# Kernel optimization log

Hardware: AMD Instinct MI355X
Metric: run time of the kernel (lower is better)

The kernel has to match this reference:

```python
import jax, jax.numpy as jnp
import numpy as np

B, L, DM = 4, 512, 512
NH, DK, DV = 8, 64, 64  # NOTE: module's view puts d_k as the 'heads' axis, n_head as feature axis
EPS = 1e-6


def setup_inputs() -> dict:
    key = jax.random.key(0)
    ks = jax.random.split(key, 12)
    xav = lambda k, shp: jax.random.uniform(k, shp, jnp.float32, -1.0, 1.0) * np.sqrt(6.0 / (shp[0] + shp[1]))
    return {
        "q": jax.random.normal(ks[0], (B, L, DM), jnp.float32),
        "k": jax.random.normal(ks[1], (B, L, DM), jnp.float32),
        "v": jax.random.normal(ks[2], (B, L, DM), jnp.float32),
        "similarity": jax.random.normal(ks[3], (B, DK, L, L), jnp.float32),
        "Wq": xav(ks[4], (NH * DK, DM)),
        "Wk": xav(ks[5], (NH * DK, DM)),
        "Wv": xav(ks[6], (NH * DV, DM)),
        "Wfc": xav(ks[7], (DM, NH * DV)),
        "bfc": jnp.zeros((DM,), jnp.float32),
        "ln_g": jnp.ones((DM,), jnp.float32),
        "ln_b": jnp.zeros((DM,), jnp.float32),
    }


def reference(q, k, v, similarity, Wq, Wk, Wv, Wfc, bfc, ln_g, ln_b):
    b, l, dm = q.shape
    residual = q
    # pre-LayerNorm applied to q only (normalize_before=True)
    mu = jnp.mean(q, axis=-1, keepdims=True)
    var = jnp.mean(jnp.square(q - mu), axis=-1, keepdims=True)
    qn = (q - mu) / jnp.sqrt(var + EPS) * ln_g + ln_b
    # projections, then view(b, l, d_k, n_head).transpose(1,2) -> [b, d_k, l, n_head]
    Q = (qn @ Wq.T).reshape(b, l, DK, NH).transpose(0, 2, 1, 3)
    K = (k @ Wk.T).reshape(b, l, DK, NH).transpose(0, 2, 1, 3)
    V = (v @ Wv.T).reshape(b, l, DK, NH).transpose(0, 2, 1, 3)
    temp = jnp.asarray(DK ** 0.5, q.dtype)
    # bias-augmented scaled dot-product attention: scores [b, d_k, l, l]
    scores = jnp.einsum('bhqe,bhke->bhqk', Q, K) / temp + similarity
    attn = jax.nn.softmax(scores, axis=-1)  # dropout omitted (eval mode)
    out = jnp.einsum('bhqk,bhke->bhqe', attn, V)  # [b, d_k, l, n_head]
    out = out.transpose(0, 2, 1, 3).reshape(b, l, DK * NH)
    out = out @ Wfc.T + bfc + residual
    return out, attn
```

## Files before the change

kernel.cpp:

```cpp
#include <hip/hip_runtime.h>

#define DMODEL 512
#define LSEQ   512
#define BATCH  4
#define NTOK   2048

typedef __attribute__((ext_vector_type(8))) short bf8;
typedef __attribute__((ext_vector_type(4))) float f4;
typedef __attribute__((ext_vector_type(4))) unsigned short us4;
typedef __attribute__((ext_vector_type(8))) unsigned short us8;

__device__ __forceinline__ unsigned short bf16_rne(float f) {
  unsigned int u = __float_as_uint(f);
  u += 0x7FFFu + ((u >> 16) & 1u);
  return (unsigned short)(u >> 16);
}
__device__ __forceinline__ void split2(float f, unsigned short& h, unsigned short& l) {
  unsigned short hh = bf16_rne(f);
  float fh = __uint_as_float(((unsigned int)hh) << 16);
  h = hh;
  l = bf16_rne(f - fh);
}

__global__ __launch_bounds__(256) void ln_kernel(const float* __restrict__ q,
    const float* __restrict__ gamma, const float* __restrict__ beta,
    unsigned short* __restrict__ qh, unsigned short* __restrict__ qlo) {
  int row = blockIdx.x;
  const float* x = q + (size_t)row * DMODEL;
  int t = threadIdx.x;
  float v0 = x[t];
  float v1 = x[t + 256];
  float s  = v0 + v1;
  float ss = v0 * v0 + v1 * v1;
  #pragma unroll
  for (int o = 32; o >= 1; o >>= 1) {
    s  += __shfl_down(s, o);
    ss += __shfl_down(ss, o);
  }
  __shared__ float ls[4], lss[4];
  __shared__ float smu, srstd;
  int wid = t >> 6, lane = t & 63;
  if (lane == 0) { ls[wid] = s; lss[wid] = ss; }
  __syncthreads();
  if (t == 0) {
    float S  = ls[0] + ls[1] + ls[2] + ls[3];
    float SS = lss[0] + lss[1] + lss[2] + lss[3];
    float mu  = S * (1.0f / DMODEL);
    float var = SS * (1.0f / DMODEL) - mu * mu;
    smu = mu;
    srstd = rsqrtf(var + 1e-6f);
  }
  __syncthreads();
  float mu = smu, rstd = srstd;
  float n0 = (v0 - mu) * rstd * gamma[t]       + beta[t];
  float n1 = (v1 - mu) * rstd * gamma[t + 256] + beta[t + 256];
  unsigned short h, l;
  size_t base = (size_t)row * DMODEL;
  split2(n0, h, l); qh[base + t] = h;       qlo[base + t] = l;
  split2(n1, h, l); qh[base + t + 256] = h; qlo[base + t + 256] = l;
}

__global__ __launch_bounds__(256) void conv_kernel(
    const float* __restrict__ k, const float* __restrict__ v,
    const float* __restrict__ Wq, const float* __restrict__ Wk,
    const float* __restrict__ Wv, const float* __restrict__ Wf,
    unsigned short* __restrict__ kh, unsigned short* __restrict__ kl,
    unsigned short* __restrict__ vh, unsigned short* __restrict__ vl,
    unsigned short* __restrict__ Wqh, unsigned short* __restrict__ Wql,
    unsigned short* __restrict__ Wkh, unsigned short* __restrict__ Wkl,
    unsigned short* __restrict__ Wvh, unsigned short* __restrict__ Wvl,
    unsigned short* __restrict__ Wfh, unsigned short* __restrict__ Wfl) {
  const float* src; unsigned short* dh; unsigned short* dl; int n;
  switch (blockIdx.y) {
    case 0:  src = k;  dh = kh;  dl = kl;  n = NTOK * DMODEL; break;
    case 1:  src = v;  dh = vh;  dl = vl;  n = NTOK * DMODEL; break;
    case 2:  src = Wq; dh = Wqh; dl = Wql; n = DMODEL * DMODEL; break;
    case 3:  src = Wk; dh = Wkh; dl = Wkl; n = DMODEL * DMODEL; break;
    case 4:  src = Wv; dh = Wvh; dl = Wvl; n = DMODEL * DMODEL; break;
    default: src = Wf; dh = Wfh; dl = Wfl; n = DMODEL * DMODEL; break;
  }
  int idx = blockIdx.x * 1024 + threadIdx.x * 4;
  if (idx >= n) return;
  float4 f = *(const float4*)(src + idx);
  us4 oh, ol;
  unsigned short h, l;
  split2(f.x, h, l); oh[0] = h; ol[0] = l;
  split2(f.y, h, l); oh[1] = h; ol[1] = l;
  split2(f.z, h, l); oh[2] = h; ol[2] = l;
  split2(f.w, h, l); oh[3] = h; ol[3] = l;
  *(us4*)(dh + idx) = oh;
  *(us4*)(dl + idx) = ol;
}

__device__ __forceinline__ void mfma_gemm_body(
    const unsigned short* __restrict__ Ah, const unsigned short* __restrict__ Al,
    const unsigned short* __restrict__ Wh, const unsigned short* __restrict__ Wl,
    float* __restrict__ C, const float* __restrict__ bias, const float* __restrict__ resid) {
  const int t = threadIdx.x;
  const int w = t >> 6, lane = t & 63;
  const int wm = w >> 1, wn = w & 1;
  const int r0 = blockIdx.y * 64 + wm * 32;
  const int c0 = blockIdx.x * 64 + wn * 32;
  const int lr = lane & 15, quad = lane >> 4;
  f4 acc[2][2] = {};
  for (int k0 = 0; k0 < DMODEL; k0 += 32) {
    const int ko = k0 + quad * 8;
    bf8 ah[2], al[2], bh[2], bl[2];
    #pragma unroll
    for (int mi = 0; mi < 2; mi++) {
      const size_t off = (size_t)(r0 + mi * 16 + lr) * DMODEL + ko;
      ah[mi] = *(const bf8*)(Ah + off);
      al[mi] = *(const bf8*)(Al + off);
    }
    #pragma unroll
    for (int ni = 0; ni < 2; ni++) {
      const size_t off = (size_t)(c0 + ni * 16 + lr) * DMODEL + ko;
      bh[ni] = *(const bf8*)(Wh + off);
      bl[ni] = *(const bf8*)(Wl + off);
    }
    #pragma unroll
    for (int mi = 0; mi < 2; mi++)
      #pragma unroll
      for (int ni = 0; ni < 2; ni++) {
        acc[mi][ni] = __builtin_amdgcn_mfma_f32_16x16x32_bf16(al[mi], bh[ni], acc[mi][ni], 0, 0, 0);
        acc[mi][ni] = __builtin_amdgcn_mfma_f32_16x16x32_bf16(ah[mi], bl[ni], acc[mi][ni], 0, 0, 0);
        acc[mi][ni] = __builtin_amdgcn_mfma_f32_16x16x32_bf16(ah[mi], bh[ni], acc[mi][ni], 0, 0, 0);
      }
  }
  #pragma unroll
  for (int mi = 0; mi < 2; mi++)
    #pragma unroll
    for (int ni = 0; ni < 2; ni++)
      #pragma unroll
      for (int r = 0; r < 4; r++) {
        int row = r0 + mi * 16 + quad * 4 + r;
        int col = c0 + ni * 16 + lr;
        float o = acc[mi][ni][r];
        if (bias)  o += bias[col];
        if (resid) o += resid[(size_t)row * DMODEL + col];
        C[(size_t)row * DMODEL + col] = o;
      }
}

__global__ __launch_bounds__(256) void proj_mfma(
    const unsigned short* __restrict__ qnh, const unsigned short* __restrict__ qnl,
    const unsigned short* __restrict__ kh, const unsigned short* __restrict__ kl,
    const unsigned short* __restrict__ vh, const unsigned short* __restrict__ vl,
    const unsigned short* __restrict__ Wqh, const unsigned short* __restrict__ Wql,
    const unsigned short* __restrict__ Wkh, const unsigned short* __restrict__ Wkl,
    const unsigned short* __restrict__ Wvh, const unsigned short* __restrict__ Wvl,
    float* __restrict__ Qp, float* __restrict__ Kp, float* __restrict__ Vp) {
  const unsigned short *Ah, *Al, *Wh, *Wl; float* C;
  if (blockIdx.z == 0)      { Ah = qnh; Al = qnl; Wh = Wqh; Wl = Wql; C = Qp; }
  else if (blockIdx.z == 1) { Ah = kh;  Al = kl;  Wh = Wkh; Wl = Wkl; C = Kp; }
  else                      { Ah = vh;  Al = vl;  Wh = Wvh; Wl = Wvl; C = Vp; }
  mfma_gemm_body(Ah, Al, Wh, Wl, C, nullptr, nullptr);
}

__global__ __launch_bounds__(256) void fc_mfma(
    const unsigned short* __restrict__ AOh, const unsigned short* __restrict__ AOl,
    const unsigned short* __restrict__ Wfh, const unsigned short* __restrict__ Wfl,
    const float* __restrict__ bfc, const float* __restrict__ resid,
    float* __restrict__ out) {
  mfma_gemm_body(AOh, AOl, Wfh, Wfl, out, bfc, resid);
}

__global__ __launch_bounds__(256, 3) void attn2_kernel(
    const float* __restrict__ Qp, const float* __restrict__ Kp, const float* __restrict__ Vp,
    const float* __restrict__ sim, float* __restrict__ attn_out,
    unsigned short* __restrict__ AOh, unsigned short* __restrict__ AOl) {
  __shared__ float Vt[8][516];
  __shared__ float Qs[64][8];
  const int qt = blockIdx.x, dk = blockIdx.y, b = blockIdx.z;
  const int t = threadIdx.x;
  const float* Vbase = Vp + (size_t)b * LSEQ * DMODEL + dk * 8;
  #pragma unroll
  for (int it = 0; it < 16; it++) {
    int idx = it * 256 + t;
    int l = idx >> 3, j = idx & 7;
    Vt[j][l] = Vbase[(size_t)l * DMODEL + j];
  }
  const float* Qbase = Qp + ((size_t)b * LSEQ + qt * 64) * DMODEL + dk * 8;
  #pragma unroll
  for (int it = 0; it < 2; it++) {
    int idx = it * 256 + t;
    int l = idx >> 3, j = idx & 7;
    Qs[l][j] = Qbase[(size_t)l * DMODEL + j];
  }
  const int lane = t & 63, w = t >> 6;
  const float* Kbase = Kp + (size_t)b * LSEQ * DMODEL + dk * 8;
  float Kr[2][8][4];
  #pragma unroll
  for (int c = 0; c < 2; c++)
    #pragma unroll
    for (int s = 0; s < 4; s++) {
      const float* kr = Kbase + (size_t)(c * 256 + lane * 4 + s) * DMODEL;
      float4 a  = *(const float4*)kr;
      float4 bb = *(const float4*)(kr + 4);
      Kr[c][0][s] = a.x;  Kr[c][1][s] = a.y;  Kr[c][2][s] = a.z;  Kr[c][3][s] = a.w;
      Kr[c][4][s] = bb.x; Kr[c][5][s] = bb.y; Kr[c][6][s] = bb.z; Kr[c][7][s] = bb.w;
    }
  __syncthreads();

  for (int qi = 0; qi < 16; qi++) {
    const int ql = w * 16 + qi;
    const int q  = qt * 64 + ql;
    const size_t rowoff = (((size_t)(b * 64 + dk) * LSEQ) + q) * LSEQ;
    float4 sv0 = *(const float4*)(sim + rowoff + lane * 4);
    float4 sv1 = *(const float4*)(sim + rowoff + 256 + lane * 4);
    float svf[2][4] = {{sv0.x, sv0.y, sv0.z, sv0.w}, {sv1.x, sv1.y, sv1.z, sv1.w}};
    float qreg[8];
    #pragma unroll
    for (int j = 0; j < 8; j++) qreg[j] = Qs[ql][j];
    float sc[2][4];
    #pragma unroll
    for (int c = 0; c < 2; c++)
      #pragma unroll
      for (int s = 0; s < 4; s++) {
        float d = 0.0f;
        #pragma unroll
        for (int j = 0; j < 8; j++) d = fmaf(qreg[j], Kr[c][j][s], d);
        sc[c][s] = fmaf(d, 0.125f, svf[c][s]);
      }
    float m = sc[0][0];
    #pragma unroll
    for (int c = 0; c < 2; c++)
      #pragma unroll
      for (int s = 0; s < 4; s++) m = fmaxf(m, sc[c][s]);
    #pragma unroll
    for (int o = 1; o < 64; o <<= 1) m = fmaxf(m, __shfl_xor(m, o));
    float p[2][4]; float sum = 0.0f;
    #pragma unroll
    for (int c = 0; c < 2; c++)
      #pragma unroll
      for (int s = 0; s < 4; s++) { p[c][s] = __expf(sc[c][s] - m); sum += p[c][s]; }
    #pragma unroll
    for (int o = 1; o < 64; o <<= 1) sum += __shfl_xor(sum, o);
    const float r = 1.0f / sum;
    #pragma unroll
    for (int c = 0; c < 2; c++)
      #pragma unroll
      for (int s = 0; s < 4; s++) p[c][s] *= r;
    float4 st0 = {p[0][0], p[0][1], p[0][2], p[0][3]};
    float4 st1 = {p[1][0], p[1][1], p[1][2], p[1][3]};
    *(float4*)(attn_out + rowoff + lane * 4) = st0;
    *(float4*)(attn_out + rowoff + 256 + lane * 4) = st1;
    float pv[8];
    #pragma unroll
    for (int j = 0; j < 8; j++) {
      float acc = 0.0f;
      #pragma unroll
      for (int c = 0; c < 2; c++) {
        float4 vv = *(const float4*)&Vt[j][c * 256 + lane * 4];
        acc = fmaf(p[c][0], vv.x, acc);
        acc = fmaf(p[c][1], vv.y, acc);
        acc = fmaf(p[c][2], vv.z, acc);
        acc = fmaf(p[c][3], vv.w, acc);
      }
      pv[j] = acc;
    }
    #pragma unroll
    for (int j = 0; j < 8; j++)
      #pragma unroll
      for (int o = 1; o < 64; o <<= 1) pv[j] += __shfl_xor(pv[j], o);
    if (lane < 2) {
      us8 ov;
      #pragma unroll
      for (int j = 0; j < 8; j++) {
        unsigned short h, l;
        split2(pv[j], h, l);
        ov[j] = (lane == 0) ? h : l;
      }
      unsigned short* dst = ((lane == 0) ? AOh : AOl) + ((size_t)b * LSEQ + q) * DMODEL + dk * 8;
      *(us8*)dst = ov;
    }
  }
}

extern "C" void kernel_launch(void* const* d_in, const int* in_sizes, int n_in,
                              void* d_out, int out_size, void* d_ws, size_t ws_size,
                              hipStream_t stream) {
  const float* q    = (const float*)d_in[0];
  const float* k    = (const float*)d_in[1];
  const float* v    = (const float*)d_in[2];
  const float* sim  = (const float*)d_in[3];
  const float* Wq   = (const float*)d_in[4];
  const float* Wk   = (const float*)d_in[5];
  const float* Wv   = (const float*)d_in[6];
  const float* Wfc  = (const float*)d_in[7];
  const float* bfc  = (const float*)d_in[8];
  const float* ln_g = (const float*)d_in[9];
  const float* ln_b = (const float*)d_in[10];

  float* out  = (float*)d_out;
  float* attn = out + (size_t)NTOK * DMODEL;

  unsigned short* kh = (unsigned short*)attn;
  unsigned short* kl = kh + (size_t)NTOK * DMODEL;
  unsigned short* vh = kl + (size_t)NTOK * DMODEL;
  unsigned short* vl = vh + (size_t)NTOK * DMODEL;
  float* Qp = out;

  unsigned short* qnh = (unsigned short*)d_ws;
  unsigned short* qnl = qnh + (size_t)NTOK * DMODEL;
  unsigned short* Wqh = qnl + (size_t)NTOK * DMODEL;
  unsigned short* Wql = Wqh + DMODEL * DMODEL;
  unsigned short* Wkh = Wql + DMODEL * DMODEL;
  unsigned short* Wkl = Wkh + DMODEL * DMODEL;
  unsigned short* Wvh = Wkl + DMODEL * DMODEL;
  unsigned short* Wvl = Wvh + DMODEL * DMODEL;
  unsigned short* Wfh = Wvl + DMODEL * DMODEL;
  unsigned short* Wfl = Wfh + DMODEL * DMODEL;
  float* Kp = (float*)(Wfl + DMODEL * DMODEL);
  float* Vp = Kp + (size_t)NTOK * DMODEL;
  unsigned short* AOh = qnh;
  unsigned short* AOl = qnl;

  ln_kernel<<<dim3(NTOK), dim3(256), 0, stream>>>(q, ln_g, ln_b, qnh, qnl);
  conv_kernel<<<dim3(1024, 6), dim3(256), 0, stream>>>(k, v, Wq, Wk, Wv, Wfc,
      kh, kl, vh, vl, Wqh, Wql, Wkh, Wkl, Wvh, Wvl, Wfh, Wfl);
  proj_mfma<<<dim3(8, 32, 3), dim3(256), 0, stream>>>(qnh, qnl, kh, kl, vh, vl,
      Wqh, Wql, Wkh, Wkl, Wvh, Wvl, Qp, Kp, Vp);
  attn2_kernel<<<dim3(8, 64, 4), dim3(256), 0, stream>>>(Qp, Kp, Vp, sim, attn, AOh, AOl);
  fc_mfma<<<dim3(8, 32, 1), dim3(256), 0, stream>>>(AOh, AOl, Wfh, Wfl, bfc, q, out);
}
```

Before: 582.4 us.

## Pair queries in attention, butterfly PV reduction, prefetch GEMM operands, smaller FC tiles

The attention loop now handles two query rows per iteration, so the K registers and V shared-memory loads serve both rows. The eight separate 64-lane PV reductions become a transpose-style butterfly in which each lane ends up owning one output column, which cuts the shuffle count. Similarity and attention traffic switches to nontemporal loads and stores. The MFMA GEMM is templated on tile size and double-buffers its global operand loads in registers, and the FC GEMM uses 32x32 tiles to launch more blocks. The cost is higher register pressure in both kernels, which could lower occupancy.

```diff
diff --git a/kernel.cpp b/kernel.cpp
--- a/kernel.cpp
+++ b/kernel.cpp
@@ -8,7 +8,6 @@
 typedef __attribute__((ext_vector_type(8))) short bf8;
 typedef __attribute__((ext_vector_type(4))) float f4;
 typedef __attribute__((ext_vector_type(4))) unsigned short us4;
-typedef __attribute__((ext_vector_type(8))) unsigned short us8;
 
 __device__ __forceinline__ unsigned short bf16_rne(float f) {
   unsigned int u = __float_as_uint(f);
@@ -92,6 +91,7 @@
   *(us4*)(dl + idx) = ol;
 }
 
+template<int TM, int TN>
 __device__ __forceinline__ void mfma_gemm_body(
     const unsigned short* __restrict__ Ah, const unsigned short* __restrict__ Al,
     const unsigned short* __restrict__ Wh, const unsigned short* __restrict__ Wl,
@@ -99,38 +99,57 @@
   const int t = threadIdx.x;
   const int w = t >> 6, lane = t & 63;
   const int wm = w >> 1, wn = w & 1;
-  const int r0 = blockIdx.y * 64 + wm * 32;
-  const int c0 = blockIdx.x * 64 + wn * 32;
+  const int r0 = blockIdx.y * (32 * TM) + wm * (16 * TM);
+  const int c0 = blockIdx.x * (32 * TN) + wn * (16 * TN);
   const int lr = lane & 15, quad = lane >> 4;
-  f4 acc[2][2] = {};
-  for (int k0 = 0; k0 < DMODEL; k0 += 32) {
-    const int ko = k0 + quad * 8;
-    bf8 ah[2], al[2], bh[2], bl[2];
-    #pragma unroll
-    for (int mi = 0; mi < 2; mi++) {
+  f4 acc[TM][TN] = {};
+  bf8 ah[2][TM], al[2][TM], bh[2][TN], bl[2][TN];
+  {
+    const int ko = quad * 8;
+    #pragma unroll
+    for (int mi = 0; mi < TM; mi++) {
       const size_t off = (size_t)(r0 + mi * 16 + lr) * DMODEL + ko;
-      ah[mi] = *(const bf8*)(Ah + off);
-      al[mi] = *(const bf8*)(Al + off);
-    }
-    #pragma unroll
-    for (int ni = 0; ni < 2; ni++) {
+      ah[0][mi] = *(const bf8*)(Ah + off);
+      al[0][mi] = *(const bf8*)(Al + off);
+    }
+    #pragma unroll
+    for (int ni = 0; ni < TN; ni++) {
       const size_t off = (size_t)(c0 + ni * 16 + lr) * DMODEL + ko;
-      bh[ni] = *(const bf8*)(Wh + off);
-      bl[ni] = *(const bf8*)(Wl + off);
-    }
-    #pragma unroll
-    for (int mi = 0; mi < 2; mi++)
-      #pragma unroll
-      for (int ni = 0; ni < 2; ni++) {
-        acc[mi][ni] = __builtin_amdgcn_mfma_f32_16x16x32_bf16(al[mi], bh[ni], acc[mi][ni], 0, 0, 0);
-        acc[mi][ni] = __builtin_amdgcn_mfma_f32_16x16x32_bf16(ah[mi], bl[ni], acc[mi][ni], 0, 0, 0);
-        acc[mi][ni] = __builtin_amdgcn_mfma_f32_16x16x32_bf16(ah[mi], bh[ni], acc[mi][ni], 0, 0, 0);
-      }
-  }
-  #pragma unroll
-  for (int mi = 0; mi < 2; mi++)
-    #pragma unroll
-    for (int ni = 0; ni < 2; ni++)
+      bh[0][ni] = *(const bf8*)(Wh + off);
+      bl[0][ni] = *(const bf8*)(Wl + off);
+    }
+  }
+  #pragma unroll
+  for (int ks = 0; ks < 16; ks++) {
+    const int cur = ks & 1, nxt = cur ^ 1;
+    if (ks < 15) {
+      const int ko = (ks + 1) * 32 + quad * 8;
+      #pragma unroll
+      for (int mi = 0; mi < TM; mi++) {
+        const size_t off = (size_t)(r0 + mi * 16 + lr) * DMODEL + ko;
+        ah[nxt][mi] = *(const bf8*)(Ah + off);
+        al[nxt][mi] = *(const bf8*)(Al + off);
+      }
+      #pragma unroll
+      for (int ni = 0; ni < TN; ni++) {
+        const size_t off = (size_t)(c0 + ni * 16 + lr) * DMODEL + ko;
+        bh[nxt][ni] = *(const bf8*)(Wh + off);
+        bl[nxt][ni] = *(const bf8*)(Wl + off);
+      }
+    }
+    #pragma unroll
+    for (int mi = 0; mi < TM; mi++)
+      #pragma unroll
+      for (int ni = 0; ni < TN; ni++) {
+        acc[mi][ni] = __builtin_amdgcn_mfma_f32_16x16x32_bf16(al[cur][mi], bh[cur][ni], acc[mi][ni], 0, 0, 0);
+        acc[mi][ni] = __builtin_amdgcn_mfma_f32_16x16x32_bf16(ah[cur][mi], bl[cur][ni], acc[mi][ni], 0, 0, 0);
+        acc[mi][ni] = __builtin_amdgcn_mfma_f32_16x16x32_bf16(ah[cur][mi], bh[cur][ni], acc[mi][ni], 0, 0, 0);
+      }
+  }
+  #pragma unroll
+  for (int mi = 0; mi < TM; mi++)
+    #pragma unroll
+    for (int ni = 0; ni < TN; ni++)
       #pragma unroll
       for (int r = 0; r < 4; r++) {
         int row = r0 + mi * 16 + quad * 4 + r;
@@ -154,7 +173,7 @@
   if (blockIdx.z == 0)      { Ah = qnh; Al = qnl; Wh = Wqh; Wl = Wql; C = Qp; }
   else if (blockIdx.z == 1) { Ah = kh;  Al = kl;  Wh = Wkh; Wl = Wkl; C = Kp; }
   else                      { Ah = vh;  Al = vl;  Wh = Wvh; Wl = Wvl; C = Vp; }
-  mfma_gemm_body(Ah, Al, Wh, Wl, C, nullptr, nullptr);
+  mfma_gemm_body<2, 2>(Ah, Al, Wh, Wl, C, nullptr, nullptr);
 }
 
 __global__ __launch_bounds__(256) void fc_mfma(
@@ -162,7 +181,31 @@
     const unsigned short* __restrict__ Wfh, const unsigned short* __restrict__ Wfl,
     const float* __restrict__ bfc, const float* __restrict__ resid,
     float* __restrict__ out) {
-  mfma_gemm_body(AOh, AOl, Wfh, Wfl, out, bfc, resid);
+  mfma_gemm_body<1, 1>(AOh, AOl, Wfh, Wfl, out, bfc, resid);
+}
+
+__device__ __forceinline__ float pv_reduce8(float pv[8], int lane) {
+  #pragma unroll
+  for (int i = 0; i < 4; i++) {
+    float sendv = (lane & 1) ? pv[i] : pv[i + 4];
+    float recv = __shfl_xor(sendv, 1);
+    pv[i] = ((lane & 1) ? pv[i + 4] : pv[i]) + recv;
+  }
+  #pragma unroll
+  for (int i = 0; i < 2; i++) {
+    float sendv = (lane & 2) ? pv[i] : pv[i + 2];
+    float recv = __shfl_xor(sendv, 2);
+    pv[i] = ((lane & 2) ? pv[i + 2] : pv[i]) + recv;
+  }
+  {
+    float sendv = (lane & 4) ? pv[0] : pv[1];
+    float recv = __shfl_xor(sendv, 4);
+    pv[0] = ((lane & 4) ? pv[1] : pv[0]) + recv;
+  }
+  pv[0] += __shfl_xor(pv[0], 8);
+  pv[0] += __shfl_xor(pv[0], 16);
+  pv[0] += __shfl_xor(pv[0], 32);
+  return pv[0];
 }
 
 __global__ __launch_bounds__(256, 3) void attn2_kernel(
@@ -202,77 +245,101 @@
     }
   __syncthreads();
 
-  for (int qi = 0; qi < 16; qi++) {
-    const int ql = w * 16 + qi;
-    const int q  = qt * 64 + ql;
-    const size_t rowoff = (((size_t)(b * 64 + dk) * LSEQ) + q) * LSEQ;
-    float4 sv0 = *(const float4*)(sim + rowoff + lane * 4);
-    float4 sv1 = *(const float4*)(sim + rowoff + 256 + lane * 4);
-    float svf[2][4] = {{sv0.x, sv0.y, sv0.z, sv0.w}, {sv1.x, sv1.y, sv1.z, sv1.w}};
-    float qreg[8];
-    #pragma unroll
-    for (int j = 0; j < 8; j++) qreg[j] = Qs[ql][j];
-    float sc[2][4];
+  for (int qp = 0; qp < 8; qp++) {
+    const int qlA = w * 16 + qp * 2;
+    const int qA = qt * 64 + qlA;
+    const size_t rowA = (((size_t)(b * 64 + dk) * LSEQ) + qA) * LSEQ;
+    const size_t rowB = rowA + LSEQ;
+    f4 sA0 = __builtin_nontemporal_load((const f4*)(sim + rowA + lane * 4));
+    f4 sA1 = __builtin_nontemporal_load((const f4*)(sim + rowA + 256 + lane * 4));
+    f4 sB0 = __builtin_nontemporal_load((const f4*)(sim + rowB + lane * 4));
+    f4 sB1 = __builtin_nontemporal_load((const f4*)(sim + rowB + 256 + lane * 4));
+    f4 qa0 = *(const f4*)&Qs[qlA][0],     qa1 = *(const f4*)&Qs[qlA][4];
+    f4 qb0 = *(const f4*)&Qs[qlA + 1][0], qb1 = *(const f4*)&Qs[qlA + 1][4];
+    float scA[2][4], scB[2][4];
     #pragma unroll
     for (int c = 0; c < 2; c++)
       #pragma unroll
       for (int s = 0; s < 4; s++) {
-        float d = 0.0f;
+        float dA = 0.0f, dB = 0.0f;
         #pragma unroll
-        for (int j = 0; j < 8; j++) d = fmaf(qreg[j], Kr[c][j][s], d);
-        sc[c][s] = fmaf(d, 0.125f, svf[c][s]);
-      }
-    float m = sc[0][0];
+        for (int j = 0; j < 4; j++) {
+          dA = fmaf(qa0[j], Kr[c][j][s], dA);
+          dB = fmaf(qb0[j], Kr[c][j][s], dB);
+        }
+        #pragma unroll
+        for (int j = 0; j < 4; j++) {
+          dA = fmaf(qa1[j], Kr[c][j + 4][s], dA);
+          dB = fmaf(qb1[j], Kr[c][j + 4][s], dB);
+        }
+        scA[c][s] = fmaf(dA, 0.125f, (c ? sA1 : sA0)[s]);
+        scB[c][s] = fmaf(dB, 0.125f, (c ? sB1 : sB0)[s]);
+      }
+    float mA = scA[0][0], mB = scB[0][0];
     #pragma unroll
     for (int c = 0; c < 2; c++)
       #pragma unroll
-      for (int s = 0; s < 4; s++) m = fmaxf(m, sc[c][s]);
-    #pragma unroll
-    for (int o = 1; o < 64; o <<= 1) m = fmaxf(m, __shfl_xor(m, o));
-    float p[2][4]; float sum = 0.0f;
+      for (int s = 0; s < 4; s++) { mA = fmaxf(mA, scA[c][s]); mB = fmaxf(mB, scB[c][s]); }
+    #pragma unroll
+    for (int o = 1; o < 64; o <<= 1) {
+      mA = fmaxf(mA, __shfl_xor(mA, o));
+      mB = fmaxf(mB, __shfl_xor(mB, o));
+    }
+    float pA[2][4], pB[2][4];
+    float sumA = 0.0f, sumB = 0.0f;
     #pragma unroll
     for (int c = 0; c < 2; c++)
       #pragma unroll
-      for (int s = 0; s < 4; s++) { p[c][s] = __expf(sc[c][s] - m); sum += p[c][s]; }
-    #pragma unroll
-    for (int o = 1; o < 64; o <<= 1) sum += __shfl_xor(sum, o);
-    const float r = 1.0f / sum;
+      for (int s = 0; s < 4; s++) {
+        pA[c][s] = __expf(scA[c][s] - mA); sumA += pA[c][s];
+        pB[c][s] = __expf(scB[c][s] - mB); sumB += pB[c][s];
+      }
+    #pragma unroll
+    for (int o = 1; o < 64; o <<= 1) {
+      sumA += __shfl_xor(sumA, o);
+      sumB += __shfl_xor(sumB, o);
+    }
+    const float rA = 1.0f / sumA, rB = 1.0f / sumB;
     #pragma unroll
     for (int c = 0; c < 2; c++)
       #pragma unroll
-      for (int s = 0; s < 4; s++) p[c][s] *= r;
-    float4 st0 = {p[0][0], p[0][1], p[0][2], p[0][3]};
-    float4 st1 = {p[1][0], p[1][1], p[1][2], p[1][3]};
-    *(float4*)(attn_out + rowoff + lane * 4) = st0;
-    *(float4*)(attn_out + rowoff + 256 + lane * 4) = st1;
-    float pv[8];
+      for (int s = 0; s < 4; s++) { pA[c][s] *= rA; pB[c][s] *= rB; }
+    f4 stA0 = {pA[0][0], pA[0][1], pA[0][2], pA[0][3]};
+    f4 stA1 = {pA[1][0], pA[1][1], pA[1][2], pA[1][3]};
+    f4 stB0 = {pB[0][0], pB[0][1], pB[0][2], pB[0][3]};
+    f4 stB1 = {pB[1][0], pB[1][1], pB[1][2], pB[1][3]};
+    __builtin_nontemporal_store(stA0, (f4*)(attn_out + rowA + lane * 4));
+    __builtin_nontemporal_store(stA1, (f4*)(attn_out + rowA + 256 + lane * 4));
+    __builtin_nontemporal_store(stB0, (f4*)(attn_out + rowB + lane * 4));
+    __builtin_nontemporal_store(stB1, (f4*)(attn_out + rowB + 256 + lane * 4));
+    float pvA[8], pvB[8];
     #pragma unroll
     for (int j = 0; j < 8; j++) {
-      float acc = 0.0f;
-      #pragma unroll
-      for (int c = 0; c < 2; c++) {
-        float4 vv = *(const float4*)&Vt[j][c * 256 + lane * 4];
-        acc = fmaf(p[c][0], vv.x, acc);
-        acc = fmaf(p[c][1], vv.y, acc);
-        acc = fmaf(p[c][2], vv.z, acc);
-        acc = fmaf(p[c][3], vv.w, acc);
-      }
-      pv[j] = acc;
-    }
-    #pragma unroll
-    for (int j = 0; j < 8; j++)
-      #pragma unroll
-      for (int o = 1; o < 64; o <<= 1) pv[j] += __shfl_xor(pv[j], o);
-    if (lane < 2) {
-      us8 ov;
-      #pragma unroll
-      for (int j = 0; j < 8; j++) {
-        unsigned short h, l;
-        split2(pv[j], h, l);
-        ov[j] = (lane == 0) ? h : l;
-      }
-      unsigned short* dst = ((lane == 0) ? AOh : AOl) + ((size_t)b * LSEQ + q) * DMODEL + dk * 8;
-      *(us8*)dst = ov;
+      f4 v0 = *(const f4*)&Vt[j][lane * 4];
+      f4 v1 = *(const f4*)&Vt[j][256 + lane * 4];
+      float aA = 0.0f, aB = 0.0f;
+      #pragma unroll
+      for (int s = 0; s < 4; s++) {
+        aA = fmaf(pA[0][s], v0[s], aA);
+        aB = fmaf(pB[0][s], v0[s], aB);
+      }
+      #pragma unroll
+      for (int s = 0; s < 4; s++) {
+        aA = fmaf(pA[1][s], v1[s], aA);
+        aB = fmaf(pB[1][s], v1[s], aB);
+      }
+      pvA[j] = aA; pvB[j] = aB;
+    }
+    float outA = pv_reduce8(pvA, lane);
+    float outB = pv_reduce8(pvB, lane);
+    if (lane < 16) {
+      const int j = ((lane & 1) << 2) | (lane & 2) | ((lane >> 2) & 1);
+      const size_t baseA = ((size_t)b * LSEQ + qA) * DMODEL + dk * 8 + j;
+      unsigned short hA, loA, hB, loB;
+      split2(outA, hA, loA);
+      split2(outB, hB, loB);
+      if (lane < 8) { AOh[baseA] = hA;  AOh[baseA + DMODEL] = hB; }
+      else          { AOl[baseA] = loA; AOl[baseA + DMODEL] = loB; }
     }
   }
 }
@@ -322,5 +389,5 @@
   proj_mfma<<<dim3(8, 32, 3), dim3(256), 0, stream>>>(qnh, qnl, kh, kl, vh, vl,
       Wqh, Wql, Wkh, Wkl, Wvh, Wvl, Qp, Kp, Vp);
   attn2_kernel<<<dim3(8, 64, 4), dim3(256), 0, stream>>>(Qp, Kp, Vp, sim, attn, AOh, AOl);
-  fc_mfma<<<dim3(8, 32, 1), dim3(256), 0, stream>>>(AOh, AOl, Wfh, Wfl, bfc, q, out);
-}
+  fc_mfma<<<dim3(16, 64, 1), dim3(256), 0, stream>>>(AOh, AOl, Wfh, Wfl, bfc, q, out);
+}
```

Measured after the change: 824.1 us. 1.42x slower.
